# Performance work log

Hardware: AMD Instinct MI355X
Metric: run time of the kernel (lower is better)

## Reference

```python
import jax, jax.numpy as jnp
import numpy as np

NH = 8  # num_heads
CHUNK = 32  # query-block size for chunked L1 cdist


def _mlp(x, w1, b1, w2, b2, w3, b3):
    h = jax.nn.relu(x @ w1 + b1)
    h = jax.nn.relu(h @ w2 + b2)
    return h @ w3 + b3


def _split_heads(x, nh):
    # Faithful to source: reshape last dim as (d, nh) then permute -> [B, nh, S, d]
    B, S, H = x.shape
    return jnp.transpose(x.reshape(B, S, H // nh, nh), (0, 3, 1, 2))


def _cdist_l1(K, Q, chunk=CHUNK):
    # torch.cdist(K, Q, p=1): D[b,h,i,j] = sum_d |K[b,h,i,d] - Q[b,h,j,d]|
    # Chunk over query rows to bound the broadcasted |K-Q| intermediate.
    B, h, Sq, d = Q.shape
    Sk = K.shape[2]
    Qb = jnp.moveaxis(Q.reshape(B, h, Sq // chunk, chunk, d), 2, 0)  # [nb,B,h,chunk,d]

    def block(q):  # q: [B,h,chunk,d]
        return jnp.sum(jnp.abs(K[:, :, :, None, :] - q[:, :, None, :, :]), axis=-1)  # [B,h,Sk,chunk]

    D = jax.lax.map(block, Qb)  # [nb,B,h,Sk,chunk]
    return jnp.moveaxis(D, 0, 3).reshape(B, h, Sk, Sq)


def setup_inputs() -> dict:
    key = jax.random.key(0)
    ks = jax.random.split(key, 32)
    B, S, F, H, O = 4, 1024, 128, 512, 128
    s = 0.02

    def lin(i, fin, fout):
        return (jax.random.normal(ks[i], (fin, fout), jnp.float32) * s,
                jnp.zeros((fout,), jnp.float32))

    inp = {
        'KEY': jax.random.normal(ks[0], (B, S, F), jnp.float32),
        'VALUE': jax.random.normal(ks[1], (B, S, F), jnp.float32),
        'QUERY': jax.random.normal(ks[2], (B, S, F), jnp.float32),
    }
    idx = 3
    for n in ['k', 'q', 'v']:
        for li, (fin, fout) in enumerate([(F, H), (H, H), (H, H)], 1):
            w, b = lin(idx, fin, fout); idx += 1
            inp[f'W{n}_w{li}'] = w
            inp[f'W{n}_b{li}'] = b
    w, b = lin(idx, H, O)
    inp['Wo_w'] = w
    inp['Wo_b'] = b
    return inp


def reference(KEY, VALUE, QUERY,
              Wk_w1, Wk_b1, Wk_w2, Wk_b2, Wk_w3, Wk_b3,
              Wq_w1, Wq_b1, Wq_w2, Wq_b2, Wq_w3, Wq_b3,
              Wv_w1, Wv_b1, Wv_w2, Wv_b2, Wv_w3, Wv_b3,
              Wo_w, Wo_b):
    Wk = _split_heads(_mlp(KEY, Wk_w1, Wk_b1, Wk_w2, Wk_b2, Wk_w3, Wk_b3), NH)   # [B,h,Sk,d]
    Wq = _split_heads(_mlp(QUERY, Wq_w1, Wq_b1, Wq_w2, Wq_b2, Wq_w3, Wq_b3), NH)  # [B,h,Sq,d]
    Wv = _split_heads(_mlp(VALUE, Wv_w1, Wv_b1, Wv_w2, Wv_b2, Wv_w3, Wv_b3), NH)  # [B,h,Sk,d]

    D = _cdist_l1(Wk, Wq)                              # [B,h,Sk,Sq]
    attn = jax.nn.softmax(-(D * D) * 0.5, axis=1)      # softmax over HEAD axis, as in source
    out = jnp.einsum('bhik,bhij->bhjk', attn, Wv)      # [B,h,d,Sq]
    B, h, d, Sq = out.shape
    out = jnp.transpose(out, (0, 2, 1, 3)).reshape(B, d * h, Sq)  # [B,hidden,Sq]
    out = jnp.transpose(out, (0, 2, 1))                # [B,Sq,hidden]
    return out @ Wo_w + Wo_b                           # dropout = identity (eval)
```

## Files before the change

### kernel.cpp

```cpp
#include <hip/hip_runtime.h>
#include <hip/hip_bf16.h>
#include <hip/hip_fp16.h>

typedef unsigned short u16;
typedef __attribute__((ext_vector_type(8))) short short8;
typedef __attribute__((ext_vector_type(4))) float floatx4;

#define DEVI static __device__ __forceinline__

DEVI float bf2f(u16 b) { return __uint_as_float(((unsigned)b) << 16); }
DEVI u16 f2bf(float f) {
  __hip_bfloat16 h = __float2bfloat16(f);
  u16 u; __builtin_memcpy(&u, &h, 2); return u;
}

struct TransArgs {
  const float* src[10];
  u16* dst[10];
  int R[10];
  int C[10];
};

__global__ __launch_bounds__(256) void transpose_k(TransArgs t) {
  const int z = blockIdx.z;
  const float* __restrict__ src = t.src[z];
  u16* __restrict__ dst = t.dst[z];
  const int R = t.R[z], C = t.C[z];
  const int c0 = blockIdx.x * 32, r0 = blockIdx.y * 32;
  if (c0 >= C || r0 >= R) return;
  __shared__ float tile[32][33];
  const int tx = threadIdx.x & 31, ty = threadIdx.x >> 5;
  for (int i = ty; i < 32; i += 8)
    tile[i][tx] = src[(size_t)(r0 + i) * C + c0 + tx];
  __syncthreads();
  for (int i = ty; i < 32; i += 8)
    dst[(size_t)(c0 + i) * R + r0 + tx] = f2bf(tile[tx][i]);
}

struct GemmArgs {
  const void* A[3];
  const u16* WT[3];
  const float* bias[3];
  void* C[3];
};

__global__ __launch_bounds__(256) void gemm_bias_act(GemmArgs ga, int M, int N, int K,
                                                     int relu, int a_f32, int c_f32) {
  const int z = blockIdx.z;
  const void* __restrict__ A = ga.A[z];
  const u16* __restrict__ WT = ga.WT[z];
  const float* __restrict__ bias = ga.bias[z];
  void* __restrict__ C = ga.C[z];

  __shared__ u16 As[64][72];
  __shared__ u16 Bs[64][72];

  const int tid = threadIdx.x;
  const int lane = tid & 63;
  const int wave = tid >> 6;
  const int wm = wave >> 1, wn = wave & 1;
  const int mb = blockIdx.y, nb = blockIdx.x;

  floatx4 acc0 = {0.f, 0.f, 0.f, 0.f}, acc1 = acc0, acc2 = acc0, acc3 = acc0;

  const int sr = tid >> 3;
  const int sc = (tid & 7) * 8;

  for (int k0 = 0; k0 < K; k0 += 64) {
    __syncthreads();
#pragma unroll
    for (int it = 0; it < 2; ++it) {
      const int rr = sr + it * 32;
      if (a_f32) {
        const float* Af = (const float*)A;
        const float4 f0 = *(const float4*)(Af + (size_t)(mb * 64 + rr) * K + k0 + sc);
        const float4 f1 = *(const float4*)(Af + (size_t)(mb * 64 + rr) * K + k0 + sc + 4);
        u16 tmp[8] = {f2bf(f0.x), f2bf(f0.y), f2bf(f0.z), f2bf(f0.w),
                      f2bf(f1.x), f2bf(f1.y), f2bf(f1.z), f2bf(f1.w)};
        int4 t; __builtin_memcpy(&t, tmp, 16);
        *(int4*)&As[rr][sc] = t;
      } else {
        const u16* Ab = (const u16*)A;
        *(int4*)&As[rr][sc] = *(const int4*)(Ab + (size_t)(mb * 64 + rr) * K + k0 + sc);
      }
      *(int4*)&Bs[rr][sc] = *(const int4*)(WT + (size_t)(nb * 64 + rr) * K + k0 + sc);
    }
    __syncthreads();
#pragma unroll
    for (int ks = 0; ks < 2; ++ks) {
      const int koff = ks * 32 + (lane >> 4) * 8;
      const int am = wm * 32 + (lane & 15);
      const int bn = wn * 32 + (lane & 15);
      short8 a0 = *(const short8*)&As[am][koff];
      short8 a1 = *(const short8*)&As[am + 16][koff];
      short8 b0 = *(const short8*)&Bs[bn][koff];
      short8 b1 = *(const short8*)&Bs[bn + 16][koff];
      acc0 = __builtin_amdgcn_mfma_f32_16x16x32_bf16(a0, b0, acc0, 0, 0, 0);
      acc1 = __builtin_amdgcn_mfma_f32_16x16x32_bf16(a0, b1, acc1, 0, 0, 0);
      acc2 = __builtin_amdgcn_mfma_f32_16x16x32_bf16(a1, b0, acc2, 0, 0, 0);
      acc3 = __builtin_amdgcn_mfma_f32_16x16x32_bf16(a1, b1, acc3, 0, 0, 0);
    }
  }

  const int colb = nb * 64 + wn * 32 + (lane & 15);
  const int rowb = mb * 64 + wm * 32 + (lane >> 4) * 4;
  const floatx4 accs[4] = {acc0, acc1, acc2, acc3};
#pragma unroll
  for (int mg = 0; mg < 2; ++mg) {
#pragma unroll
    for (int ng = 0; ng < 2; ++ng) {
      const int col = colb + ng * 16;
      const float bv = bias[col];
      const floatx4 v = accs[mg * 2 + ng];
#pragma unroll
      for (int r = 0; r < 4; ++r) {
        const int row = rowb + mg * 16 + r;
        float x = v[r] + bv;
        if (relu) x = fmaxf(x, 0.f);
        if (c_f32) ((float*)C)[(size_t)row * N + col] = x;
        else       ((u16*)C)[(size_t)row * N + col] = f2bf(x);
      }
    }
  }
}

DEVI int4 bf8_to_h8(int4 raw) {
  const u16* u = reinterpret_cast<const u16*>(&raw);
  int4 out;
  __half* h = reinterpret_cast<__half*>(&out);
#pragma unroll
  for (int i = 0; i < 8; ++i)
    h[i] = __float2half(__uint_as_float(((unsigned)u[i]) << 16));
  return out;
}

__global__ __launch_bounds__(256) void attn_kernel(const u16* __restrict__ Km,
                                                   const u16* __restrict__ Qm,
                                                   const u16* __restrict__ Vm,
                                                   float* __restrict__ partial) {
  __shared__ alignas(16) u16 Qs[16 * 512];
  __shared__ alignas(16) u16 Ks[16 * 512];
  __shared__ alignas(16) u16 Vs[16 * 512];
  __shared__ alignas(16) u16 attn_h[16 * 16 * 8];

  const int tid = threadIdx.x;
  const int lane = tid & 63;
  const int wave = tid >> 6;
  const int bid = blockIdx.x;
  const int qt = bid & 63;
  const int sp = (bid >> 6) & 1;
  const int b = bid >> 7;
  const int j0 = qt * 16;

  for (int s = tid; s < 1024; s += 256) {
    const int r = s >> 6, gg = s & 63;
    const int4 raw = *(const int4*)(Qm + ((size_t)(b * 1024 + j0 + r) * 512) + gg * 8);
    *(int4*)(Qs + r * 512 + ((gg ^ (r & 7)) * 8)) = bf8_to_h8(raw);
  }

  const int key = lane & 15;
  const int quad = lane >> 4;
  const int q_local = wave * 4 + quad;
  const int ksw = key & 7;
  const int qsw = q_local & 7;
  const int g = lane;

  int koff8[8], qoff8[8], voff8[8];
#pragma unroll
  for (int t = 0; t < 8; ++t) {
    koff8[t] = key * 512 + ((ksw ^ t) * 8);
    qoff8[t] = q_local * 512 + ((qsw ^ t) * 8);
    voff8[t] = (g ^ t) * 8;
  }

  float o[32];
#pragma unroll
  for (int i = 0; i < 32; ++i) o[i] = 0.f;

#pragma unroll 1
  for (int chunk = 0; chunk < 32; ++chunk) {
    __syncthreads();
    const int i0 = sp * 512 + chunk * 16;
    for (int s = tid; s < 1024; s += 256) {
      const int r = s >> 6, gg = s & 63;
      const size_t goff = ((size_t)(b * 1024 + i0 + r) * 512) + gg * 8;
      const int4 kraw = *(const int4*)(Km + goff);
      const int4 vraw = *(const int4*)(Vm + goff);
      const int sw = (gg ^ (r & 7)) * 8;
      *(int4*)(Ks + r * 512 + sw) = bf8_to_h8(kraw);
      *(int4*)(Vs + r * 512 + sw) = bf8_to_h8(vraw);
    }
    __syncthreads();

    float d8[8];
#pragma unroll
    for (int h = 0; h < 8; ++h) d8[h] = 0.f;

#pragma unroll
    for (int gb = 0; gb < 4; ++gb) {
      __half2 a0 = __float2half2_rn(0.f), a1 = a0, a2 = a0, a3 = a0;
#pragma unroll
      for (int gh = 0; gh < 2; ++gh) {
        const int ghi = gb * 2 + gh;
#pragma unroll
        for (int glo = 0; glo < 8; ++glo) {
          const int4 kv = *(const int4*)(Ks + koff8[glo] + ghi * 64);
          const int4 qv = *(const int4*)(Qs + qoff8[glo] + ghi * 64);
          const __half2* kh = reinterpret_cast<const __half2*>(&kv);
          const __half2* qh = reinterpret_cast<const __half2*>(&qv);
          a0 = __hadd2(a0, __habs2(__hsub2(kh[0], qh[0])));
          a1 = __hadd2(a1, __habs2(__hsub2(kh[1], qh[1])));
          a2 = __hadd2(a2, __habs2(__hsub2(kh[2], qh[2])));
          a3 = __hadd2(a3, __habs2(__hsub2(kh[3], qh[3])));
        }
      }
      const float2 f0 = __half22float2(a0), f1 = __half22float2(a1);
      const float2 f2 = __half22float2(a2), f3 = __half22float2(a3);
      d8[0] += f0.x; d8[1] += f0.y; d8[2] += f1.x; d8[3] += f1.y;
      d8[4] += f2.x; d8[5] += f2.y; d8[6] += f3.x; d8[7] += f3.y;
    }

    float p[8];
#pragma unroll
    for (int h = 0; h < 8; ++h) p[h] = d8[h] * d8[h];
    float m = p[0];
#pragma unroll
    for (int h = 1; h < 8; ++h) m = fminf(m, p[h]);
    float w[8], norm = 0.f;
#pragma unroll
    for (int h = 0; h < 8; ++h) { w[h] = __expf(0.5f * (m - p[h])); norm += w[h]; }
    const float inv = 1.0f / norm;
    int4 wpack;
    __half2* wh = reinterpret_cast<__half2*>(&wpack);
    wh[0] = __floats2half2_rn(w[0] * inv, w[1] * inv);
    wh[1] = __floats2half2_rn(w[2] * inv, w[3] * inv);
    wh[2] = __floats2half2_rn(w[4] * inv, w[5] * inv);
    wh[3] = __floats2half2_rn(w[6] * inv, w[7] * inv);
    *(int4*)&attn_h[(q_local * 16 + key) * 8] = wpack;

    __half2 oa[4][4];
#pragma unroll
    for (int q = 0; q < 4; ++q)
#pragma unroll
      for (int i = 0; i < 4; ++i) oa[q][i] = __float2half2_rn(0.f);

#pragma unroll
    for (int k2 = 0; k2 < 16; ++k2) {
      const int4 vv = *(const int4*)(Vs + voff8[k2 & 7] + k2 * 512);
      const __half2* vh = reinterpret_cast<const __half2*>(&vv);
#pragma unroll
      for (int q = 0; q < 4; ++q) {
        const int4 av = *(const int4*)&attn_h[((wave * 4 + q) * 16 + k2) * 8];
        const __half2* ah = reinterpret_cast<const __half2*>(&av);
        oa[q][0] = __hfma2(ah[0], vh[0], oa[q][0]);
        oa[q][1] = __hfma2(ah[1], vh[1], oa[q][1]);
        oa[q][2] = __hfma2(ah[2], vh[2], oa[q][2]);
        oa[q][3] = __hfma2(ah[3], vh[3], oa[q][3]);
      }
    }
#pragma unroll
    for (int q = 0; q < 4; ++q)
#pragma unroll
      for (int i = 0; i < 4; ++i) {
        const float2 f = __half22float2(oa[q][i]);
        o[q * 8 + i * 2] += f.x;
        o[q * 8 + i * 2 + 1] += f.y;
      }
  }

#pragma unroll
  for (int q = 0; q < 4; ++q) {
    const int j = j0 + wave * 4 + q;
    float* dst = partial + ((size_t)sp * 4096 + b * 1024 + j) * 512 + g * 8;
    *(float4*)dst = make_float4(o[q * 8 + 0], o[q * 8 + 1], o[q * 8 + 2], o[q * 8 + 3]);
    *(float4*)(dst + 4) = make_float4(o[q * 8 + 4], o[q * 8 + 5], o[q * 8 + 6], o[q * 8 + 7]);
  }
}

__global__ __launch_bounds__(256) void reduce_k(const float* __restrict__ p,
                                                u16* __restrict__ out) {
  const size_t i = (size_t)blockIdx.x * 256 + threadIdx.x;
  const float4 a0 = *(const float4*)(p + i * 8);
  const float4 a1 = *(const float4*)(p + i * 8 + 4);
  const float4 b0 = *(const float4*)(p + 2097152 + i * 8);
  const float4 b1 = *(const float4*)(p + 2097152 + i * 8 + 4);
  int4 pk;
  u16* pu = reinterpret_cast<u16*>(&pk);
  pu[0] = f2bf(a0.x + b0.x); pu[1] = f2bf(a0.y + b0.y);
  pu[2] = f2bf(a0.z + b0.z); pu[3] = f2bf(a0.w + b0.w);
  pu[4] = f2bf(a1.x + b1.x); pu[5] = f2bf(a1.y + b1.y);
  pu[6] = f2bf(a1.z + b1.z); pu[7] = f2bf(a1.w + b1.w);
  *(int4*)(out + i * 8) = pk;
}

extern "C" void kernel_launch(void* const* d_in, const int* in_sizes, int n_in,
                              void* d_out, int out_size, void* d_ws, size_t ws_size,
                              hipStream_t stream) {
  (void)in_sizes; (void)n_in; (void)out_size; (void)ws_size;
  char* wsp = (char*)d_ws;
  size_t off = 0;
  auto take = [&](size_t bytes) {
    void* p = (void*)(wsp + off);
    off += ((bytes + 255) & ~(size_t)255);
    return p;
  };

  static const int wR[10] = {128, 512, 512, 128, 512, 512, 128, 512, 512, 512};
  static const int wC[10] = {512, 512, 512, 512, 512, 512, 512, 512, 512, 128};
  static const int widx[10] = {3, 5, 7, 9, 11, 13, 15, 17, 19, 21};

  u16* WT[10];
  for (int i = 0; i < 10; ++i) WT[i] = (u16*)take((size_t)wR[i] * wC[i] * 2);
  u16* h1[3]; for (int i = 0; i < 3; ++i) h1[i] = (u16*)take((size_t)4096 * 512 * 2);
  u16* h2[3]; for (int i = 0; i < 3; ++i) h2[i] = (u16*)take((size_t)4096 * 512 * 2);
  float* partial = (float*)take((size_t)2 * 4096 * 512 * 4);

  TransArgs ta;
  for (int i = 0; i < 10; ++i) {
    ta.src[i] = (const float*)d_in[widx[i]];
    ta.dst[i] = WT[i];
    ta.R[i] = wR[i];
    ta.C[i] = wC[i];
  }
  hipLaunchKernelGGL(transpose_k, dim3(16, 16, 10), dim3(256), 0, stream, ta);

  GemmArgs g1 = {};
  g1.A[0] = d_in[0]; g1.A[1] = d_in[2]; g1.A[2] = d_in[1];
  g1.WT[0] = WT[0]; g1.WT[1] = WT[3]; g1.WT[2] = WT[6];
  g1.bias[0] = (const float*)d_in[4]; g1.bias[1] = (const float*)d_in[10]; g1.bias[2] = (const float*)d_in[16];
  g1.C[0] = h1[0]; g1.C[1] = h1[1]; g1.C[2] = h1[2];
  hipLaunchKernelGGL(gemm_bias_act, dim3(8, 64, 3), dim3(256), 0, stream, g1, 4096, 512, 128, 1, 1, 0);

  GemmArgs g2 = {};
  for (int i = 0; i < 3; ++i) { g2.A[i] = h1[i]; g2.C[i] = h2[i]; }
  g2.WT[0] = WT[1]; g2.WT[1] = WT[4]; g2.WT[2] = WT[7];
  g2.bias[0] = (const float*)d_in[6]; g2.bias[1] = (const float*)d_in[12]; g2.bias[2] = (const float*)d_in[18];
  hipLaunchKernelGGL(gemm_bias_act, dim3(8, 64, 3), dim3(256), 0, stream, g2, 4096, 512, 512, 1, 0, 0);

  GemmArgs g3 = {};
  for (int i = 0; i < 3; ++i) { g3.A[i] = h2[i]; g3.C[i] = h1[i]; }
  g3.WT[0] = WT[2]; g3.WT[1] = WT[5]; g3.WT[2] = WT[8];
  g3.bias[0] = (const float*)d_in[8]; g3.bias[1] = (const float*)d_in[14]; g3.bias[2] = (const float*)d_in[20];
  hipLaunchKernelGGL(gemm_bias_act, dim3(8, 64, 3), dim3(256), 0, stream, g3, 4096, 512, 512, 0, 0, 0);

  hipLaunchKernelGGL(attn_kernel, dim3(512), dim3(256), 0, stream, h1[0], h1[1], h1[2], partial);

  hipLaunchKernelGGL(reduce_k, dim3(1024), dim3(256), 0, stream, partial, h2[0]);

  GemmArgs g4 = {};
  g4.A[0] = h2[0]; g4.WT[0] = WT[9]; g4.bias[0] = (const float*)d_in[22]; g4.C[0] = d_out;
  hipLaunchKernelGGL(gemm_bias_act, dim3(2, 64, 1), dim3(256), 0, stream, g4, 4096, 128, 512, 0, 0, 1);
}
```

Baseline: 416.8 us.

## Restructure attention kernel with register-resident queries and per-wave key slices

Each wave now owns its own slice of 128 keys and keeps its block's 16 query rows in registers as fp16. The L1 distance is reduced across 8 lanes with xor shuffles instead of a shared attention-weight buffer. This removes the block-wide syncs per chunk and the Q loads from LDS. Output accumulators stay in fp16 registers across all keys, and the four waves' partial outputs are combined through LDS at the end. The costs are heavy register pressure (a 2-wave launch bound), more fp16 accumulation error over 128 keys per wave, and a serial cross-wave reduction at the end.

```diff
diff --git a/kernel.cpp b/kernel.cpp
--- a/kernel.cpp
+++ b/kernel.cpp
@@ -134,14 +134,18 @@
   return out;
 }
 
-__global__ __launch_bounds__(256) void attn_kernel(const u16* __restrict__ Km,
-                                                   const u16* __restrict__ Qm,
-                                                   const u16* __restrict__ Vm,
-                                                   float* __restrict__ partial) {
-  __shared__ alignas(16) u16 Qs[16 * 512];
-  __shared__ alignas(16) u16 Ks[16 * 512];
-  __shared__ alignas(16) u16 Vs[16 * 512];
-  __shared__ alignas(16) u16 attn_h[16 * 16 * 8];
+DEVI __half2 shfl_xor_h2(__half2 v, int m) {
+  int i; __builtin_memcpy(&i, &v, 4);
+  i = __shfl_xor(i, m, 64);
+  __half2 r; __builtin_memcpy(&r, &i, 4);
+  return r;
+}
+
+__global__ __launch_bounds__(256, 2) void attn_kernel(const u16* __restrict__ Km,
+                                                      const u16* __restrict__ Qm,
+                                                      const u16* __restrict__ Vm,
+                                                      float* __restrict__ partial) {
+  __shared__ alignas(16) u16 lds[4][2][8 * 512];
 
   const int tid = threadIdx.x;
   const int lane = tid & 63;
@@ -151,129 +155,157 @@
   const int sp = (bid >> 6) & 1;
   const int b = bid >> 7;
   const int j0 = qt * 16;
-
-  for (int s = tid; s < 1024; s += 256) {
-    const int r = s >> 6, gg = s & 63;
-    const int4 raw = *(const int4*)(Qm + ((size_t)(b * 1024 + j0 + r) * 512) + gg * 8);
-    *(int4*)(Qs + r * 512 + ((gg ^ (r & 7)) * 8)) = bf8_to_h8(raw);
-  }
-
-  const int key = lane & 15;
-  const int quad = lane >> 4;
-  const int q_local = wave * 4 + quad;
-  const int ksw = key & 7;
-  const int qsw = q_local & 7;
-  const int g = lane;
-
-  int koff8[8], qoff8[8], voff8[8];
-#pragma unroll
-  for (int t = 0; t < 8; ++t) {
-    koff8[t] = key * 512 + ((ksw ^ t) * 8);
-    qoff8[t] = q_local * 512 + ((qsw ^ t) * 8);
-    voff8[t] = (g ^ t) * 8;
-  }
-
-  float o[32];
-#pragma unroll
-  for (int i = 0; i < 32; ++i) o[i] = 0.f;
+  const int qg = lane >> 3;
+  const int s = lane & 7;
+
+  int4 Qreg[2][8];
+#pragma unroll
+  for (int qi = 0; qi < 2; ++qi) {
+    const u16* qrow = Qm + (size_t)(b * 1024 + j0 + qg + qi * 8) * 512;
+#pragma unroll
+    for (int pi = 0; pi < 8; ++pi)
+      Qreg[qi][pi] = bf8_to_h8(*(const int4*)(qrow + (s * 8 + pi) * 8));
+  }
+
+  __half2 o[2][8][4];
+#pragma unroll
+  for (int qi = 0; qi < 2; ++qi)
+#pragma unroll
+    for (int pi = 0; pi < 8; ++pi)
+#pragma unroll
+      for (int j = 0; j < 4; ++j) o[qi][pi][j] = __float2half2_rn(0.f);
+
+  u16* Kw = &lds[wave][0][0];
+  u16* Vw = &lds[wave][1][0];
+  const int keyBase = b * 1024 + sp * 512 + wave * 128;
+  const int phys = (lane & 56) | ((lane ^ (lane >> 3)) & 7);
 
 #pragma unroll 1
-  for (int chunk = 0; chunk < 32; ++chunk) {
-    __syncthreads();
-    const int i0 = sp * 512 + chunk * 16;
-    for (int s = tid; s < 1024; s += 256) {
-      const int r = s >> 6, gg = s & 63;
-      const size_t goff = ((size_t)(b * 1024 + i0 + r) * 512) + gg * 8;
-      const int4 kraw = *(const int4*)(Km + goff);
-      const int4 vraw = *(const int4*)(Vm + goff);
-      const int sw = (gg ^ (r & 7)) * 8;
-      *(int4*)(Ks + r * 512 + sw) = bf8_to_h8(kraw);
-      *(int4*)(Vs + r * 512 + sw) = bf8_to_h8(vraw);
-    }
-    __syncthreads();
-
-    float d8[8];
-#pragma unroll
-    for (int h = 0; h < 8; ++h) d8[h] = 0.f;
-
-#pragma unroll
-    for (int gb = 0; gb < 4; ++gb) {
-      __half2 a0 = __float2half2_rn(0.f), a1 = a0, a2 = a0, a3 = a0;
-#pragma unroll
-      for (int gh = 0; gh < 2; ++gh) {
-        const int ghi = gb * 2 + gh;
-#pragma unroll
-        for (int glo = 0; glo < 8; ++glo) {
-          const int4 kv = *(const int4*)(Ks + koff8[glo] + ghi * 64);
-          const int4 qv = *(const int4*)(Qs + qoff8[glo] + ghi * 64);
-          const __half2* kh = reinterpret_cast<const __half2*>(&kv);
-          const __half2* qh = reinterpret_cast<const __half2*>(&qv);
-          a0 = __hadd2(a0, __habs2(__hsub2(kh[0], qh[0])));
-          a1 = __hadd2(a1, __habs2(__hsub2(kh[1], qh[1])));
-          a2 = __hadd2(a2, __habs2(__hsub2(kh[2], qh[2])));
-          a3 = __hadd2(a3, __habs2(__hsub2(kh[3], qh[3])));
+  for (int c = 0; c < 16; ++c) {
+    const int row0 = keyBase + c * 8;
+#pragma unroll
+    for (int r = 0; r < 8; ++r) {
+      const size_t ga = (size_t)(row0 + r) * 512 + lane * 8;
+      const int4 kr = *(const int4*)(Km + ga);
+      const int4 vr = *(const int4*)(Vm + ga);
+      *(int4*)(Kw + r * 512 + phys * 8) = bf8_to_h8(kr);
+      *(int4*)(Vw + r * 512 + phys * 8) = bf8_to_h8(vr);
+    }
+
+#pragma unroll 1
+    for (int kk = 0; kk < 8; ++kk) {
+      const u16* krow = Kw + kk * 512;
+      __half2 acc[2][4];
+#pragma unroll
+      for (int qi = 0; qi < 2; ++qi)
+#pragma unroll
+        for (int j = 0; j < 4; ++j) acc[qi][j] = __float2half2_rn(0.f);
+
+#pragma unroll
+      for (int pi = 0; pi < 8; ++pi) {
+        const int4 kv = *(const int4*)(krow + (s * 8 + (pi ^ s)) * 8);
+        const __half2* kh = reinterpret_cast<const __half2*>(&kv);
+#pragma unroll
+        for (int qi = 0; qi < 2; ++qi) {
+          const __half2* qh = reinterpret_cast<const __half2*>(&Qreg[qi][pi]);
+          acc[qi][0] = __hadd2(acc[qi][0], __habs2(__hsub2(kh[0], qh[0])));
+          acc[qi][1] = __hadd2(acc[qi][1], __habs2(__hsub2(kh[1], qh[1])));
+          acc[qi][2] = __hadd2(acc[qi][2], __habs2(__hsub2(kh[2], qh[2])));
+          acc[qi][3] = __hadd2(acc[qi][3], __habs2(__hsub2(kh[3], qh[3])));
         }
       }
-      const float2 f0 = __half22float2(a0), f1 = __half22float2(a1);
-      const float2 f2 = __half22float2(a2), f3 = __half22float2(a3);
-      d8[0] += f0.x; d8[1] += f0.y; d8[2] += f1.x; d8[3] += f1.y;
-      d8[4] += f2.x; d8[5] += f2.y; d8[6] += f3.x; d8[7] += f3.y;
-    }
-
-    float p[8];
-#pragma unroll
-    for (int h = 0; h < 8; ++h) p[h] = d8[h] * d8[h];
-    float m = p[0];
-#pragma unroll
-    for (int h = 1; h < 8; ++h) m = fminf(m, p[h]);
-    float w[8], norm = 0.f;
-#pragma unroll
-    for (int h = 0; h < 8; ++h) { w[h] = __expf(0.5f * (m - p[h])); norm += w[h]; }
-    const float inv = 1.0f / norm;
-    int4 wpack;
-    __half2* wh = reinterpret_cast<__half2*>(&wpack);
-    wh[0] = __floats2half2_rn(w[0] * inv, w[1] * inv);
-    wh[1] = __floats2half2_rn(w[2] * inv, w[3] * inv);
-    wh[2] = __floats2half2_rn(w[4] * inv, w[5] * inv);
-    wh[3] = __floats2half2_rn(w[6] * inv, w[7] * inv);
-    *(int4*)&attn_h[(q_local * 16 + key) * 8] = wpack;
-
-    __half2 oa[4][4];
-#pragma unroll
-    for (int q = 0; q < 4; ++q)
-#pragma unroll
-      for (int i = 0; i < 4; ++i) oa[q][i] = __float2half2_rn(0.f);
-
-#pragma unroll
-    for (int k2 = 0; k2 < 16; ++k2) {
-      const int4 vv = *(const int4*)(Vs + voff8[k2 & 7] + k2 * 512);
-      const __half2* vh = reinterpret_cast<const __half2*>(&vv);
-#pragma unroll
-      for (int q = 0; q < 4; ++q) {
-        const int4 av = *(const int4*)&attn_h[((wave * 4 + q) * 16 + k2) * 8];
-        const __half2* ah = reinterpret_cast<const __half2*>(&av);
-        oa[q][0] = __hfma2(ah[0], vh[0], oa[q][0]);
-        oa[q][1] = __hfma2(ah[1], vh[1], oa[q][1]);
-        oa[q][2] = __hfma2(ah[2], vh[2], oa[q][2]);
-        oa[q][3] = __hfma2(ah[3], vh[3], oa[q][3]);
-      }
-    }
-#pragma unroll
-    for (int q = 0; q < 4; ++q)
-#pragma unroll
-      for (int i = 0; i < 4; ++i) {
-        const float2 f = __half22float2(oa[q][i]);
-        o[q * 8 + i * 2] += f.x;
-        o[q * 8 + i * 2 + 1] += f.y;
-      }
-  }
-
-#pragma unroll
-  for (int q = 0; q < 4; ++q) {
-    const int j = j0 + wave * 4 + q;
-    float* dst = partial + ((size_t)sp * 4096 + b * 1024 + j) * 512 + g * 8;
-    *(float4*)dst = make_float4(o[q * 8 + 0], o[q * 8 + 1], o[q * 8 + 2], o[q * 8 + 3]);
-    *(float4*)(dst + 4) = make_float4(o[q * 8 + 4], o[q * 8 + 5], o[q * 8 + 6], o[q * 8 + 7]);
+#pragma unroll
+      for (int m = 1; m < 8; m <<= 1)
+#pragma unroll
+        for (int qi = 0; qi < 2; ++qi)
+#pragma unroll
+          for (int j = 0; j < 4; ++j)
+            acc[qi][j] = __hadd2(acc[qi][j], shfl_xor_h2(acc[qi][j], m));
+
+      __half2 w[2][4];
+#pragma unroll
+      for (int qi = 0; qi < 2; ++qi) {
+        float p[8];
+#pragma unroll
+        for (int j = 0; j < 4; ++j) {
+          const float2 f = __half22float2(acc[qi][j]);
+          p[j * 2] = f.x * f.x;
+          p[j * 2 + 1] = f.y * f.y;
+        }
+        float mn = p[0];
+#pragma unroll
+        for (int h = 1; h < 8; ++h) mn = fminf(mn, p[h]);
+        float wg[8], norm = 0.f;
+#pragma unroll
+        for (int h = 0; h < 8; ++h) { wg[h] = __expf(0.5f * (mn - p[h])); norm += wg[h]; }
+        const float inv = 1.0f / norm;
+        w[qi][0] = __floats2half2_rn(wg[0] * inv, wg[1] * inv);
+        w[qi][1] = __floats2half2_rn(wg[2] * inv, wg[3] * inv);
+        w[qi][2] = __floats2half2_rn(wg[4] * inv, wg[5] * inv);
+        w[qi][3] = __floats2half2_rn(wg[6] * inv, wg[7] * inv);
+      }
+
+      const u16* vrow = Vw + kk * 512;
+#pragma unroll
+      for (int pi = 0; pi < 8; ++pi) {
+        const int4 vv = *(const int4*)(vrow + (s * 8 + (pi ^ s)) * 8);
+        const __half2* vh = reinterpret_cast<const __half2*>(&vv);
+#pragma unroll
+        for (int qi = 0; qi < 2; ++qi) {
+          o[qi][pi][0] = __hfma2(w[qi][0], vh[0], o[qi][pi][0]);
+          o[qi][pi][1] = __hfma2(w[qi][1], vh[1], o[qi][pi][1]);
+          o[qi][pi][2] = __hfma2(w[qi][2], vh[2], o[qi][pi][2]);
+          o[qi][pi][3] = __hfma2(w[qi][3], vh[3], o[qi][pi][3]);
+        }
+      }
+    }
+  }
+
+  u16* red = &lds[0][0][0];
+  auto store_o = [&](u16* rg) {
+#pragma unroll
+    for (int qi = 0; qi < 2; ++qi)
+#pragma unroll
+      for (int pi = 0; pi < 8; ++pi) {
+        int4 t; __builtin_memcpy(&t, &o[qi][pi][0], 16);
+        *(int4*)(rg + ((qi * 8 + pi) * 64 + lane) * 8) = t;
+      }
+  };
+  auto add_o = [&](const u16* rg) {
+#pragma unroll
+    for (int qi = 0; qi < 2; ++qi)
+#pragma unroll
+      for (int pi = 0; pi < 8; ++pi) {
+        const int4 t = *(const int4*)(rg + ((qi * 8 + pi) * 64 + lane) * 8);
+        const __half2* th = reinterpret_cast<const __half2*>(&t);
+#pragma unroll
+        for (int j = 0; j < 4; ++j) o[qi][pi][j] = __hadd2(o[qi][pi][j], th[j]);
+      }
+  };
+
+  __syncthreads();
+  if (wave >= 2) store_o(red + (wave - 2) * 8192);
+  __syncthreads();
+  if (wave < 2) add_o(red + wave * 8192);
+  __syncthreads();
+  if (wave == 1) store_o(red + 2 * 8192);
+  __syncthreads();
+  if (wave == 0) {
+    add_o(red + 2 * 8192);
+#pragma unroll
+    for (int qi = 0; qi < 2; ++qi) {
+      const int j = j0 + qg + qi * 8;
+      float* dst = partial + ((size_t)sp * 4096 + b * 1024 + j) * 512 + s * 64;
+#pragma unroll
+      for (int pi = 0; pi < 8; ++pi) {
+        const float2 f0 = __half22float2(o[qi][pi][0]);
+        const float2 f1 = __half22float2(o[qi][pi][1]);
+        const float2 f2 = __half22float2(o[qi][pi][2]);
+        const float2 f3 = __half22float2(o[qi][pi][3]);
+        *(float4*)(dst + pi * 8) = make_float4(f0.x, f0.y, f1.x, f1.y);
+        *(float4*)(dst + pi * 8 + 4) = make_float4(f2.x, f2.y, f3.x, f3.y);
+      }
+    }
   }
 }
 
```

Result: slower. 446.5 us (+7.1%).
